# Kernel optimization log

Hardware: AMD Instinct MI355X
Metric: run time of the kernel (lower is better)

The kernel has to match this reference:

```python
import jax, jax.numpy as jnp
import numpy as np
import math

B, S, D = 1, 4096, 2048
H, KVH, HD = 16, 4, 128
ROPE_THETA = 10000.0


def _rope_tables(seq_len, head_dim, theta):
    inv_freq = 1.0 / (theta ** (jnp.arange(0, head_dim, 2, dtype=jnp.float32) / head_dim))
    t = jnp.arange(seq_len, dtype=jnp.float32)
    freqs = jnp.outer(t, inv_freq)                      # [S, HD/2]
    emb = jnp.concatenate([freqs, freqs], axis=-1)      # [S, HD]
    return jnp.cos(emb)[None, None], jnp.sin(emb)[None, None]  # [1,1,S,HD]


def setup_inputs() -> dict:
    key = jax.random.key(0)
    ks = jax.random.split(key, 8)
    hidden_states = jax.random.normal(ks[0], (B, S, D), dtype=jnp.float32)
    # additive causal mask [B,1,S,S]
    neg = jnp.finfo(jnp.float32).min
    causal = jnp.where(jnp.tril(jnp.ones((S, S), dtype=bool)), 0.0, neg)
    attention_mask = jnp.broadcast_to(causal[None, None], (B, 1, S, S)).astype(jnp.float32)
    cos, sin = _rope_tables(S, HD, ROPE_THETA)
    gate = jax.random.uniform(ks[1], (B, S), dtype=jnp.float32, minval=0.05, maxval=1.0)
    sc = lambda fan_in: 1.0 / math.sqrt(fan_in)
    Wq = jax.random.normal(ks[2], (D, H * HD), dtype=jnp.float32) * sc(D)
    Wk = jax.random.normal(ks[3], (D, KVH * HD), dtype=jnp.float32) * sc(D)
    Wv = jax.random.normal(ks[4], (D, KVH * HD), dtype=jnp.float32) * sc(D)
    Wo = jax.random.normal(ks[5], (H * HD, D), dtype=jnp.float32) * sc(H * HD)
    return {"hidden_states": hidden_states, "attention_mask": attention_mask,
            "cos": cos, "sin": sin, "gate": gate,
            "Wq": Wq, "Wk": Wk, "Wv": Wv, "Wo": Wo}


def _rotate_half(x):
    h = x.shape[-1] // 2
    return jnp.concatenate([-x[..., h:], x[..., :h]], axis=-1)


def reference(hidden_states, attention_mask, cos, sin, gate, Wq, Wk, Wv, Wo):
    bsz, q_len, _ = hidden_states.shape
    # projections -> [B, heads, S, HD]
    q = (hidden_states @ Wq).reshape(bsz, q_len, H, HD).transpose(0, 2, 1, 3)
    k = (hidden_states @ Wk).reshape(bsz, q_len, KVH, HD).transpose(0, 2, 1, 3)
    v = (hidden_states @ Wv).reshape(bsz, q_len, KVH, HD).transpose(0, 2, 1, 3)
    # inline RoPE
    q = q * cos + _rotate_half(q) * sin
    k = k * cos + _rotate_half(k) * sin
    # GQA: repeat-interleave kv heads to match q heads
    g = H // KVH
    k = jnp.repeat(k, g, axis=1)
    v = jnp.repeat(v, g, axis=1)
    scores = jnp.einsum('bhqd,bhkd->bhqk', q, k) / math.sqrt(HD)
    scores = scores + attention_mask
    scores = scores + jnp.log(gate + 1e-8)[:, None, None, :]  # gate over kv positions
    weights = jax.nn.softmax(scores.astype(jnp.float32), axis=-1).astype(q.dtype)
    out = jnp.einsum('bhqk,bhkd->bhqd', weights, v)
    out = out.transpose(0, 2, 1, 3).reshape(bsz, q_len, H * HD)
    return out @ Wo
```

## Files before the change

kernel.cpp:

```cpp
#include <hip/hip_runtime.h>
#include <math.h>

#define S_LEN 4096
#define DMODEL 2048
#define NH 16
#define NKVH 4
#define HD 128
#define LDQKV 3072

typedef __attribute__((ext_vector_type(4))) float f32x4;
typedef __attribute__((ext_vector_type(8))) short bf16x8;
typedef __attribute__((ext_vector_type(8))) unsigned short us8;
typedef __attribute__((ext_vector_type(4))) unsigned short us4;

static __device__ __forceinline__ unsigned short f2bf(float f) {
  unsigned int u = __builtin_bit_cast(unsigned int, f);
  u += 0x7fffu + ((u >> 16) & 1u);
  return (unsigned short)(u >> 16);
}
static __device__ __forceinline__ float bf2f(unsigned short h) {
  unsigned int u = ((unsigned int)h) << 16;
  return __builtin_bit_cast(float, u);
}
static __device__ __forceinline__ unsigned int cvt_pk_bf16(float lo, float hi) {
  unsigned int r;
  asm("v_cvt_pk_bf16_f32 %0, %1, %2" : "=v"(r) : "v"(lo), "v"(hi));
  return r;
}

#define GLDS16(g, l) __builtin_amdgcn_global_load_lds( \
    (__attribute__((address_space(1))) void*)(g), \
    (__attribute__((address_space(3))) void*)(l), 16, 0, 0)


__global__ __launch_bounds__(256) void k_prep(
    const float* __restrict__ hid, unsigned short* __restrict__ Xb,
    const float* __restrict__ Wq, const float* __restrict__ Wk,
    const float* __restrict__ Wv, const float* __restrict__ Wo,
    unsigned short* __restrict__ Wt, unsigned short* __restrict__ Wot) {
  __shared__ float tile[64][65];
  const int b = blockIdx.x, t = threadIdx.x;
  if (b < 8192) {
    int i = b * 256 + t;
    const float4* s = (const float4*)hid;
    float4 v = s[i];
    us4 o = { f2bf(v.x), f2bf(v.y), f2bf(v.z), f2bf(v.w) };
    *(us4*)(Xb + (size_t)i * 4) = o;
    return;
  }
  const int bb = b - 8192;
  const float* src;
  unsigned short* dst;
  int N, c;
  if (bb < 1024)      { src = Wq; dst = Wt;                       N = 2048; c = bb; }
  else if (bb < 1280) { src = Wk; dst = Wt + (size_t)2048 * 2048; N = 512;  c = bb - 1024; }
  else if (bb < 1536) { src = Wv; dst = Wt + (size_t)2560 * 2048; N = 512;  c = bb - 1280; }
  else                { src = Wo; dst = Wot;                      N = 2048; c = bb - 1536; }
  const int k0 = (c & 31) * 64, n0 = (c >> 5) * 64;
#pragma unroll
  for (int i = 0; i < 16; ++i) {
    int idx = t + i * 256;
    int r = idx >> 6, cc = idx & 63;
    tile[r][cc] = src[(size_t)(k0 + r) * N + n0 + cc];
  }
  __syncthreads();
#pragma unroll
  for (int i = 0; i < 16; ++i) {
    int idx = t + i * 256;
    int r = idx >> 6, cc = idx & 63;
    dst[(size_t)(n0 + r) * 2048 + k0 + cc] = f2bf(tile[cc][r]);
  }
}


__global__ __launch_bounds__(256) void k_vt(
    const unsigned short* __restrict__ QKV, unsigned short* __restrict__ Vt) {
  __shared__ unsigned short tile[64][72];
  const int b = blockIdx.x, t = threadIdx.x;
  const int s0 = (b & 63) * 64, c0 = (b >> 6) * 64;
#pragma unroll
  for (int i = 0; i < 16; ++i) {
    int idx = t + i * 256;
    int r = idx >> 6, cc = idx & 63;
    tile[r][cc] = QKV[(size_t)(s0 + r) * LDQKV + DMODEL + NKVH * HD + c0 + cc];
  }
  __syncthreads();
#pragma unroll
  for (int i = 0; i < 16; ++i) {
    int idx = t + i * 256;
    int r = idx >> 6, cc = idx & 63;
    int pc = (cc & 3) * 16 + (cc >> 2);
    Vt[(size_t)(c0 + r) * S_LEN + s0 + cc] = tile[pc][r];
  }
}


template<int MODE>
__global__ __launch_bounds__(256) void k_gemm_bt(
    const unsigned short* __restrict__ A, const unsigned short* __restrict__ Bt,
    void* __restrict__ Cp, int M, int N, int K,
    const float* __restrict__ cp, const float* __restrict__ sp) {
  __shared__ __attribute__((aligned(16))) unsigned short As[128 * 32];
  __shared__ __attribute__((aligned(16))) unsigned short Bs[128 * 32];
  const int t = threadIdx.x;
  const int wave = t >> 6, lane = t & 63;
  const int lr = lane & 15, lg = lane >> 4;
  const int bm = blockIdx.x * 128, bn = blockIdx.y * 128;
  const int wr = wave * 32;
  f32x4 acc[2][8];
#pragma unroll
  for (int i = 0; i < 2; ++i)
#pragma unroll
    for (int j = 0; j < 8; ++j) acc[i][j] = (f32x4){0.f, 0.f, 0.f, 0.f};

  for (int k0 = 0; k0 < K; k0 += 32) {
    __syncthreads();
#pragma unroll
    for (int i = 0; i < 2; ++i) {
      const int cb = (wave * 2 + i) * 64;
      const int c = cb + lane;
      const int row = c >> 2, kc = c & 3;
      const int ksw = (kc ^ (row & 3)) * 8;
      GLDS16(A + (size_t)(bm + row) * K + k0 + ksw, (char*)As + cb * 16);
      GLDS16(Bt + (size_t)(bn + row) * K + k0 + ksw, (char*)Bs + cb * 16);
    }
    asm volatile("s_waitcnt vmcnt(0)" ::: "memory");
    __syncthreads();
    bf16x8 af[2], bfr[8];
#pragma unroll
    for (int mi = 0; mi < 2; ++mi) {
      const int row = wr + mi * 16 + lr;
      af[mi] = *(const bf16x8*)(As + row * 32 + ((lg ^ (lr & 3)) * 8));
    }
#pragma unroll
    for (int ni = 0; ni < 8; ++ni) {
      const int row = ni * 16 + lr;
      bfr[ni] = *(const bf16x8*)(Bs + row * 32 + ((lg ^ (lr & 3)) * 8));
    }
#pragma unroll
    for (int mi = 0; mi < 2; ++mi)
#pragma unroll
      for (int ni = 0; ni < 8; ++ni)
        acc[mi][ni] = __builtin_amdgcn_mfma_f32_16x16x32_bf16(af[mi], bfr[ni], acc[mi][ni], 0, 0, 0);
  }

  if (MODE == 1 && bn < NKVH * HD + DMODEL) {
    const float qs = bn < DMODEL ? 0.12751589341664477f : 1.0f;
    unsigned short* o = (unsigned short*)Cp;
#pragma unroll
    for (int mi = 0; mi < 2; ++mi)
#pragma unroll
      for (int r = 0; r < 4; ++r) {
        const int m = bm + wr + mi * 16 + lg * 4 + r;
#pragma unroll
        for (int ni = 0; ni < 4; ++ni) {
          const int d = ni * 16 + lr;
          const float c = cp[m * HD + d], s = sp[m * HD + d];
          const float x1 = acc[mi][ni][r], x2 = acc[mi][ni + 4][r];
          o[(size_t)m * N + bn + d]      = f2bf((x1 * c - x2 * s) * qs);
          o[(size_t)m * N + bn + d + 64] = f2bf((x2 * c + x1 * s) * qs);
        }
      }
    return;
  }
#pragma unroll
  for (int mi = 0; mi < 2; ++mi)
#pragma unroll
    for (int ni = 0; ni < 8; ++ni)
#pragma unroll
      for (int r = 0; r < 4; ++r) {
        const int m = bm + wr + mi * 16 + lg * 4 + r;
        const int n = bn + ni * 16 + lr;
        if (MODE == 2) ((float*)Cp)[(size_t)m * N + n] = acc[mi][ni][r];
        else ((unsigned short*)Cp)[(size_t)m * N + n] = f2bf(acc[mi][ni][r]);
      }
}


#define STAGE_KV(kt_, buf_) do { \
  const int kv0_ = (kt_) * 64; \
  _Pragma("unroll") \
  for (int i_ = 0; i_ < 2; ++i_) { \
    const int cb_ = (wave * 2 + i_) * 64; \
    const int c_ = cb_ + lane; \
    { const int row_ = c_ >> 4, kc_ = c_ & 15; \
      GLDS16(Kp + (size_t)(kv0_ + row_) * LDQKV + ((kc_ ^ (row_ & 7)) * 8), \
             (char*)Ks[buf_] + cb_ * 16); } \
    { const int d_ = c_ >> 3, kc_ = c_ & 7; \
      GLDS16(Vp + (size_t)d_ * S_LEN + kv0_ + ((kc_ ^ (d_ & 7)) * 8), \
             (char*)Vs[buf_] + cb_ * 16); } \
  } \
} while (0)

__global__ __launch_bounds__(512) void k_attn(
    const unsigned short* __restrict__ QKV, const unsigned short* __restrict__ Vt,
    const float* __restrict__ gate, unsigned short* __restrict__ N1,
    unsigned short* __restrict__ N2, float2* __restrict__ Ms) {
  __shared__ __attribute__((aligned(16))) unsigned short Ks[2][64 * 128];
  __shared__ __attribute__((aligned(16))) unsigned short Vs[2][128 * 64];
  __shared__ __attribute__((aligned(16))) unsigned short Ps[8][2][16][72];
  const int bx = blockIdx.x;
  const int st = 15 - (bx >> 5);
  const int rem = bx & 31;
  const int h = rem >> 1, chunk = rem & 1;
  const int kvh = h >> 2;
  const int t = threadIdx.x, wave = t >> 6, lane = t & 63;
  const int lr = lane & 15, lg = lane >> 4;
  const unsigned short* Qp = QKV + h * HD;
  const unsigned short* Kp = QKV + DMODEL + kvh * HD;
  const unsigned short* Vp = Vt + (size_t)kvh * HD * S_LEN;
  bf16x8 vb_ones;
  {
    const short one = (short)0x3F80, z = 0;
    const short e = (lr == 0) ? one : z;
    vb_ones = (bf16x8){e, e, e, e, e, e, e, e};
  }

  const int q0 = st * 256;
  const int half_nt = 2 * st + 2;
  const int kt_lo = chunk * half_nt, kt_hi = kt_lo + half_nt;
  const int qb[2] = { q0 + wave * 32 + lg * 4, q0 + wave * 32 + 16 + lg * 4 };

  bf16x8 qf[2][4];
#pragma unroll
  for (int g = 0; g < 2; ++g) {
    const size_t qoff = (size_t)(q0 + wave * 32 + g * 16 + lr) * LDQKV;
#pragma unroll
    for (int ks = 0; ks < 4; ++ks)
      qf[g][ks] = *(const bf16x8*)(Qp + qoff + ks * 32 + lg * 8);
  }
  f32x4 acc[2][8];
#pragma unroll
  for (int g = 0; g < 2; ++g)
#pragma unroll
    for (int j = 0; j < 8; ++j) acc[g][j] = (f32x4){0.f, 0.f, 0.f, 0.f};
  f32x4 acc_s[2] = { (f32x4){0.f, 0.f, 0.f, 0.f}, (f32x4){0.f, 0.f, 0.f, 0.f} };
  float mrow[2][4] = { {-3e38f, -3e38f, -3e38f, -3e38f}, {-3e38f, -3e38f, -3e38f, -3e38f} };
  f32x4 sc[2][4];
  float g4[4];

  STAGE_KV(kt_lo, kt_lo & 1);

  for (int kt = kt_lo; kt < kt_hi; ++kt) {
    const int kv0 = kt * 64;
    if (kt + 1 < kt_hi) {
      STAGE_KV(kt + 1, (kt + 1) & 1);
      asm volatile("s_waitcnt vmcnt(4)" ::: "memory");
    } else {
      asm volatile("s_waitcnt vmcnt(0)" ::: "memory");
    }
    __builtin_amdgcn_s_barrier();
    const unsigned short* Kb = Ks[kt & 1];
    const unsigned short* Vb = Vs[kt & 1];
#pragma unroll
    for (int cf = 0; cf < 4; ++cf) g4[cf] = gate[kv0 + cf * 16 + lr];

    __builtin_amdgcn_s_setprio(1);
#pragma unroll
    for (int cf = 0; cf < 4; ++cf) {
      sc[0][cf] = (f32x4){0.f, 0.f, 0.f, 0.f};
      sc[1][cf] = (f32x4){0.f, 0.f, 0.f, 0.f};
      const int row = cf * 16 + lr;
#pragma unroll
      for (int ks = 0; ks < 4; ++ks) {
        bf16x8 kb = *(const bf16x8*)(Kb + row * 128 + (((ks * 4 + lg) ^ (lr & 7)) * 8));
        sc[0][cf] = __builtin_amdgcn_mfma_f32_16x16x32_bf16(qf[0][ks], kb, sc[0][cf], 0, 0, 0);
        sc[1][cf] = __builtin_amdgcn_mfma_f32_16x16x32_bf16(qf[1][ks], kb, sc[1][cf], 0, 0, 0);
      }
    }
    __builtin_amdgcn_s_setprio(0);

    const bool tail = kv0 >= q0;
#pragma unroll
    for (int g = 0; g < 2; ++g) {
      if (tail) {
#pragma unroll
        for (int cf = 0; cf < 4; ++cf) {
          const int kpos = kv0 + cf * 16 + lr;
#pragma unroll
          for (int r = 0; r < 4; ++r)
            sc[g][cf][r] = (kpos <= qb[g] + r) ? sc[g][cf][r] : -3e38f;
        }
      }
      float lmax[4];
#pragma unroll
      for (int r = 0; r < 4; ++r)
        lmax[r] = fmaxf(fmaxf(sc[g][0][r], sc[g][1][r]), fmaxf(sc[g][2][r], sc[g][3][r]));
      bool need = (lmax[0] > mrow[g][0] + 11.5416f) | (lmax[1] > mrow[g][1] + 11.5416f) |
                  (lmax[2] > mrow[g][2] + 11.5416f) | (lmax[3] > mrow[g][3] + 11.5416f);
      if (__any(need)) {
        float tm[4] = {lmax[0], lmax[1], lmax[2], lmax[3]};
#pragma unroll
        for (int off = 8; off; off >>= 1)
#pragma unroll
          for (int r = 0; r < 4; ++r) tm[r] = fmaxf(tm[r], __shfl_xor(tm[r], off));
#pragma unroll
        for (int r = 0; r < 4; ++r) {
          const float mn = fmaxf(mrow[g][r], tm[r]);
          const float alpha = __builtin_amdgcn_exp2f(mrow[g][r] - mn);
          mrow[g][r] = mn;
#pragma unroll
          for (int j = 0; j < 8; ++j) acc[g][j][r] *= alpha;
          acc_s[g][r] *= alpha;
        }
      }
#pragma unroll
      for (int r = 0; r < 4; ++r) {
        float p0 = __builtin_amdgcn_exp2f(sc[g][0][r] - mrow[g][r]) * g4[0];
        float p1 = __builtin_amdgcn_exp2f(sc[g][1][r] - mrow[g][r]) * g4[1];
        float p2 = __builtin_amdgcn_exp2f(sc[g][2][r] - mrow[g][r]) * g4[2];
        float p3 = __builtin_amdgcn_exp2f(sc[g][3][r] - mrow[g][r]) * g4[3];
        uint2 pk = { cvt_pk_bf16(p0, p1), cvt_pk_bf16(p2, p3) };
        *(uint2*)(&Ps[wave][g][lg * 4 + r][lr * 4]) = pk;
      }
    }
    __builtin_amdgcn_s_setprio(1);
#pragma unroll
    for (int ks = 0; ks < 2; ++ks) {
      bf16x8 pa0 = *(const bf16x8*)(&Ps[wave][0][lr][ks * 32 + lg * 8]);
      bf16x8 pa1 = *(const bf16x8*)(&Ps[wave][1][lr][ks * 32 + lg * 8]);
#pragma unroll
      for (int j = 0; j < 8; ++j) {
        const int d = j * 16 + lr;
        bf16x8 vb = *(const bf16x8*)(Vb + d * 64 + (((ks * 4 + lg) ^ (lr & 7)) * 8));
        acc[0][j] = __builtin_amdgcn_mfma_f32_16x16x32_bf16(pa0, vb, acc[0][j], 0, 0, 0);
        acc[1][j] = __builtin_amdgcn_mfma_f32_16x16x32_bf16(pa1, vb, acc[1][j], 0, 0, 0);
      }
      acc_s[0] = __builtin_amdgcn_mfma_f32_16x16x32_bf16(pa0, vb_ones, acc_s[0], 0, 0, 0);
      acc_s[1] = __builtin_amdgcn_mfma_f32_16x16x32_bf16(pa1, vb_ones, acc_s[1], 0, 0, 0);
    }
    __builtin_amdgcn_s_setprio(0);
    __builtin_amdgcn_s_barrier();
  }

  unsigned short* Nd = chunk ? N2 : N1;
#pragma unroll
  for (int g = 0; g < 2; ++g) {
#pragma unroll
    for (int j = 0; j < 8; ++j)
#pragma unroll
      for (int r = 0; r < 4; ++r)
        Nd[(size_t)(qb[g] + r) * DMODEL + h * HD + j * 16 + lr] = f2bf(acc[g][j][r]);
  }
  if (lr == 0) {
#pragma unroll
    for (int g = 0; g < 2; ++g)
#pragma unroll
      for (int r = 0; r < 4; ++r)
        Ms[(size_t)(chunk * 16 + h) * S_LEN + qb[g] + r] =
            make_float2(mrow[g][r], acc_s[g][r]);
  }
}


__global__ __launch_bounds__(256) void k_comb(
    unsigned short* __restrict__ N1, const unsigned short* __restrict__ N2,
    const float2* __restrict__ Ms) {
  const int gid = blockIdx.x * 256 + threadIdx.x;
  const size_t e = (size_t)gid * 8;
  const int row = (int)(e >> 11);
  const int col = (int)(e & 2047);
  const int h = col >> 7;
  const float2 a = Ms[(size_t)h * S_LEN + row];
  const float2 b = Ms[(size_t)(16 + h) * S_LEN + row];
  const float m = fmaxf(a.x, b.x);
  const float w1 = __builtin_amdgcn_exp2f(a.x - m);
  const float w2 = __builtin_amdgcn_exp2f(b.x - m);
  const float inv = 1.0f / (w1 * a.y + w2 * b.y);
  us8 n1 = *(const us8*)(N1 + e);
  us8 n2 = *(const us8*)(N2 + e);
  us8 o;
#pragma unroll
  for (int k = 0; k < 8; ++k)
    o[k] = f2bf((w1 * bf2f(n1[k]) + w2 * bf2f(n2[k])) * inv);
  *(us8*)(N1 + e) = o;
}


extern "C" void kernel_launch(void* const* d_in, const int* in_sizes, int n_in,
                              void* d_out, int out_size, void* d_ws, size_t ws_size,
                              hipStream_t stream) {
  (void)in_sizes; (void)n_in; (void)out_size; (void)ws_size;
  const float* hid  = (const float*)d_in[0];
  const float* cosp = (const float*)d_in[2];
  const float* sinp = (const float*)d_in[3];
  const float* gate = (const float*)d_in[4];
  const float* Wq   = (const float*)d_in[5];
  const float* Wk   = (const float*)d_in[6];
  const float* Wv   = (const float*)d_in[7];
  const float* Wo   = (const float*)d_in[8];
  float* out = (float*)d_out;
  char* ws = (char*)d_ws;
  unsigned short* Xb   = (unsigned short*)(ws);
  unsigned short* Wt   = (unsigned short*)(ws + (size_t)16777216);
  unsigned short* Wot  = (unsigned short*)(ws + (size_t)29360128);
  unsigned short* QKV  = (unsigned short*)(ws + (size_t)37748736);
  unsigned short* Oatt = (unsigned short*)(ws + (size_t)62914560);
  unsigned short* Vt   = (unsigned short*)(ws + (size_t)79691776);
  unsigned short* Np   = Xb;
  float2* Ms           = (float2*)Wt;

  k_prep<<<10752, 256, 0, stream>>>(hid, Xb, Wq, Wk, Wv, Wo, Wt, Wot);
  k_gemm_bt<1><<<dim3(32, 24), 256, 0, stream>>>(Xb, Wt, QKV, 4096, 3072, 2048, cosp, sinp);
  k_vt<<<512, 256, 0, stream>>>(QKV, Vt);
  k_attn<<<512, 512, 0, stream>>>(QKV, Vt, gate, Oatt, Np, Ms);
  k_comb<<<4096, 256, 0, stream>>>(Oatt, Np, Ms);
  k_gemm_bt<2><<<dim3(32, 16), 256, 0, stream>>>(Oatt, Wot, out, 4096, 2048, 2048, nullptr, nullptr);
}
```

Baseline: 247.1 us.

## Rewrite projection GEMMs with triple-buffered 256x128 tiles and 8-wave ping-pong scheduling

Replaces the single-buffered 128x128, 4-wave GEMM with a 256x128-tile, 8-wave kernel. It uses a 3-stage LDS ring with BK=64, so global-to-LDS loads for tile k+2 overlap the MFMA work on tile k, along with s_setprio around the MFMA bursts and an XCD-aware block remapping. The goal is to hide global load latency and drop the per-iteration full vmcnt(0) stall of the old loop. The cost is 144KB of LDS, which allows one workgroup per CU, and a more intricate barrier and waitcnt protocol.

```diff
diff --git a/kernel.cpp b/kernel.cpp
--- a/kernel.cpp
+++ b/kernel.cpp
@@ -95,53 +95,91 @@
 }
 
 
+#define STG_A(kt_, buf_, j_) do { \
+  const int row_ = (j_) * 64 + srow; \
+  GLDS16(A + (size_t)(bm + row_) * K + (kt_) * 64 + ((gsel ^ (srow & 7)) * 8), \
+         (char*)Ab[buf_] + (j_) * 8192 + wave * 1024); \
+} while (0)
+#define STG_B(kt_, buf_, j_) do { \
+  const int row_ = (j_) * 64 + srow; \
+  GLDS16(Bt + (size_t)(bn + row_) * K + (kt_) * 64 + ((gsel ^ (srow & 7)) * 8), \
+         (char*)Bb[buf_] + (j_) * 8192 + wave * 1024); \
+} while (0)
+
 template<int MODE>
-__global__ __launch_bounds__(256) void k_gemm_bt(
+__global__ __launch_bounds__(512, 1) void k_gemm8(
     const unsigned short* __restrict__ A, const unsigned short* __restrict__ Bt,
-    void* __restrict__ Cp, int M, int N, int K,
+    void* __restrict__ Cp, int M, int N, int K, int nbm, int nbn,
     const float* __restrict__ cp, const float* __restrict__ sp) {
-  __shared__ __attribute__((aligned(16))) unsigned short As[128 * 32];
-  __shared__ __attribute__((aligned(16))) unsigned short Bs[128 * 32];
-  const int t = threadIdx.x;
-  const int wave = t >> 6, lane = t & 63;
+  __shared__ __attribute__((aligned(16))) unsigned short Ab[3][256 * 64];
+  __shared__ __attribute__((aligned(16))) unsigned short Bb[3][128 * 64];
+  const int t = threadIdx.x, wave = t >> 6, lane = t & 63;
   const int lr = lane & 15, lg = lane >> 4;
-  const int bm = blockIdx.x * 128, bn = blockIdx.y * 128;
+  const int srow = wave * 8 + (lane >> 3);
+  const int gsel = lane & 7;
+  const int nwg = nbm * nbn;
+  const int q8 = nwg >> 3;
+  const int wg = (blockIdx.x & 7) * q8 + (blockIdx.x >> 3);
+  const int bm = (wg % nbm) * 256, bn = (wg / nbm) * 128;
   const int wr = wave * 32;
+
   f32x4 acc[2][8];
 #pragma unroll
   for (int i = 0; i < 2; ++i)
 #pragma unroll
     for (int j = 0; j < 8; ++j) acc[i][j] = (f32x4){0.f, 0.f, 0.f, 0.f};
 
-  for (int k0 = 0; k0 < K; k0 += 32) {
-    __syncthreads();
-#pragma unroll
-    for (int i = 0; i < 2; ++i) {
-      const int cb = (wave * 2 + i) * 64;
-      const int c = cb + lane;
-      const int row = c >> 2, kc = c & 3;
-      const int ksw = (kc ^ (row & 3)) * 8;
-      GLDS16(A + (size_t)(bm + row) * K + k0 + ksw, (char*)As + cb * 16);
-      GLDS16(Bt + (size_t)(bn + row) * K + k0 + ksw, (char*)Bs + cb * 16);
-    }
-    asm volatile("s_waitcnt vmcnt(0)" ::: "memory");
-    __syncthreads();
-    bf16x8 af[2], bfr[8];
-#pragma unroll
-    for (int mi = 0; mi < 2; ++mi) {
-      const int row = wr + mi * 16 + lr;
-      af[mi] = *(const bf16x8*)(As + row * 32 + ((lg ^ (lr & 3)) * 8));
-    }
-#pragma unroll
-    for (int ni = 0; ni < 8; ++ni) {
-      const int row = ni * 16 + lr;
-      bfr[ni] = *(const bf16x8*)(Bs + row * 32 + ((lg ^ (lr & 3)) * 8));
-    }
-#pragma unroll
-    for (int mi = 0; mi < 2; ++mi)
-#pragma unroll
-      for (int ni = 0; ni < 8; ++ni)
-        acc[mi][ni] = __builtin_amdgcn_mfma_f32_16x16x32_bf16(af[mi], bfr[ni], acc[mi][ni], 0, 0, 0);
+#pragma unroll
+  for (int tt = 0; tt < 2; ++tt) {
+    STG_A(tt, tt, 0); STG_A(tt, tt, 1); STG_A(tt, tt, 2); STG_A(tt, tt, 3);
+    STG_B(tt, tt, 0); STG_B(tt, tt, 1);
+  }
+  asm volatile("s_waitcnt vmcnt(6)" ::: "memory");
+  __builtin_amdgcn_s_barrier();
+
+  const int nkt = K >> 6;
+  for (int kt = 0; kt < nkt; ++kt) {
+    const int cur = kt % 3;
+    const int nx = (kt + 2) % 3;
+    const unsigned short* Ac = Ab[cur];
+    const unsigned short* Bc = Bb[cur];
+    const bool stg = kt < nkt - 2;
+
+    bf16x8 aq[2], bq[8][2];
+#pragma unroll
+    for (int ks = 0; ks < 2; ++ks)
+      aq[ks] = *(const bf16x8*)(Ac + (wr + lr) * 64 + (((ks * 4 + lg) ^ (lr & 7)) * 8));
+#pragma unroll
+    for (int nf = 0; nf < 8; ++nf)
+#pragma unroll
+      for (int ks = 0; ks < 2; ++ks)
+        bq[nf][ks] = *(const bf16x8*)(Bc + (nf * 16 + lr) * 64 + (((ks * 4 + lg) ^ (lr & 7)) * 8));
+    if (stg) { STG_A(kt + 2, nx, 0); STG_A(kt + 2, nx, 1); STG_B(kt + 2, nx, 0); }
+    __builtin_amdgcn_s_barrier();
+    __builtin_amdgcn_s_setprio(1);
+#pragma unroll
+    for (int nf = 0; nf < 8; ++nf)
+#pragma unroll
+      for (int ks = 0; ks < 2; ++ks)
+        acc[0][nf] = __builtin_amdgcn_mfma_f32_16x16x32_bf16(aq[ks], bq[nf][ks], acc[0][nf], 0, 0, 0);
+    __builtin_amdgcn_s_setprio(0);
+    __builtin_amdgcn_s_barrier();
+
+#pragma unroll
+    for (int ks = 0; ks < 2; ++ks)
+      aq[ks] = *(const bf16x8*)(Ac + (wr + 16 + lr) * 64 + (((ks * 4 + lg) ^ (lr & 7)) * 8));
+    if (stg) { STG_A(kt + 2, nx, 2); STG_A(kt + 2, nx, 3); STG_B(kt + 2, nx, 1); }
+    __builtin_amdgcn_s_barrier();
+    __builtin_amdgcn_s_setprio(1);
+#pragma unroll
+    for (int nf = 0; nf < 8; ++nf)
+#pragma unroll
+      for (int ks = 0; ks < 2; ++ks)
+        acc[1][nf] = __builtin_amdgcn_mfma_f32_16x16x32_bf16(aq[ks], bq[nf][ks], acc[1][nf], 0, 0, 0);
+    __builtin_amdgcn_s_setprio(0);
+    if (stg)                  asm volatile("s_waitcnt vmcnt(6)" ::: "memory");
+    else if (kt == nkt - 2)   asm volatile("s_waitcnt vmcnt(0)" ::: "memory");
+    __builtin_amdgcn_s_barrier();
   }
 
   if (MODE == 1 && bn < NKVH * HD + DMODEL) {
@@ -401,9 +439,9 @@
   float2* Ms           = (float2*)Wt;
 
   k_prep<<<10752, 256, 0, stream>>>(hid, Xb, Wq, Wk, Wv, Wo, Wt, Wot);
-  k_gemm_bt<1><<<dim3(32, 24), 256, 0, stream>>>(Xb, Wt, QKV, 4096, 3072, 2048, cosp, sinp);
+  k_gemm8<1><<<384, 512, 0, stream>>>(Xb, Wt, QKV, 4096, 3072, 2048, 16, 24, cosp, sinp);
   k_vt<<<512, 256, 0, stream>>>(QKV, Vt);
   k_attn<<<512, 512, 0, stream>>>(QKV, Vt, gate, Oatt, Np, Ms);
   k_comb<<<4096, 256, 0, stream>>>(Oatt, Np, Ms);
-  k_gemm_bt<2><<<dim3(32, 16), 256, 0, stream>>>(Oatt, Wot, out, 4096, 2048, 2048, nullptr, nullptr);
-}
+  k_gemm8<2><<<256, 512, 0, stream>>>(Oatt, Wot, out, 4096, 2048, 2048, 16, 16, nullptr, nullptr);
+}
```

Measured after the change: 257.2 us. 4.1% more time.

## Fold gate into V transpose and row-sum MFMA instead of per-tile multiply

Applied to the files above, without the earlier changes.

Multiplies V by the per-position gate while building the transposed V, and writes a permuted bf16 gate array that is staged into shared memory once per attention block. The softmax denominator MFMA then uses the gate fragment in place of the ones vector, so the per-tile gate loads and per-element multiplies on probabilities are removed. In exchange, V is rounded to bf16 after gating (extra rounding), more LDS is used, and there is an extra small load per k-step.

```diff
diff --git a/kernel.cpp b/kernel.cpp
--- a/kernel.cpp
+++ b/kernel.cpp
@@ -74,23 +74,31 @@
 
 
 __global__ __launch_bounds__(256) void k_vt(
-    const unsigned short* __restrict__ QKV, unsigned short* __restrict__ Vt) {
+    const unsigned short* __restrict__ QKV, const float* __restrict__ gate,
+    unsigned short* __restrict__ Vt, unsigned short* __restrict__ garr) {
   __shared__ unsigned short tile[64][72];
   const int b = blockIdx.x, t = threadIdx.x;
-  const int s0 = (b & 63) * 64, c0 = (b >> 6) * 64;
-#pragma unroll
-  for (int i = 0; i < 16; ++i) {
-    int idx = t + i * 256;
-    int r = idx >> 6, cc = idx & 63;
-    tile[r][cc] = QKV[(size_t)(s0 + r) * LDQKV + DMODEL + NKVH * HD + c0 + cc];
-  }
-  __syncthreads();
-#pragma unroll
-  for (int i = 0; i < 16; ++i) {
-    int idx = t + i * 256;
-    int r = idx >> 6, cc = idx & 63;
-    int pc = (cc & 3) * 16 + (cc >> 2);
-    Vt[(size_t)(c0 + r) * S_LEN + s0 + cc] = tile[pc][r];
+  if (b < 512) {
+    const int s0 = (b & 63) * 64, c0 = (b >> 6) * 64;
+#pragma unroll
+    for (int i = 0; i < 16; ++i) {
+      int idx = t + i * 256;
+      int r = idx >> 6, cc = idx & 63;
+      tile[r][cc] = QKV[(size_t)(s0 + r) * LDQKV + DMODEL + NKVH * HD + c0 + cc];
+    }
+    __syncthreads();
+#pragma unroll
+    for (int i = 0; i < 16; ++i) {
+      int idx = t + i * 256;
+      int r = idx >> 6, cc = idx & 63;
+      int pc = (cc & 3) * 16 + (cc >> 2);
+      float gv = bf2f(tile[pc][r]) * gate[s0 + pc];
+      Vt[(size_t)(c0 + r) * S_LEN + s0 + cc] = f2bf(gv);
+    }
+  } else {
+    int gid = (b - 512) * 256 + t;
+    int blk = gid >> 6, c = gid & 63;
+    garr[gid] = f2bf(gate[blk * 64 + (c & 3) * 16 + (c >> 2)]);
   }
 }
 
@@ -194,11 +202,12 @@
 
 __global__ __launch_bounds__(512) void k_attn(
     const unsigned short* __restrict__ QKV, const unsigned short* __restrict__ Vt,
-    const float* __restrict__ gate, unsigned short* __restrict__ N1,
+    const unsigned short* __restrict__ garr, unsigned short* __restrict__ N1,
     unsigned short* __restrict__ N2, float2* __restrict__ Ms) {
   __shared__ __attribute__((aligned(16))) unsigned short Ks[2][64 * 128];
   __shared__ __attribute__((aligned(16))) unsigned short Vs[2][128 * 64];
   __shared__ __attribute__((aligned(16))) unsigned short Ps[8][2][16][72];
+  __shared__ __attribute__((aligned(16))) unsigned short Lg[4096];
   const int bx = blockIdx.x;
   const int st = 15 - (bx >> 5);
   const int rem = bx & 31;
@@ -209,12 +218,8 @@
   const unsigned short* Qp = QKV + h * HD;
   const unsigned short* Kp = QKV + DMODEL + kvh * HD;
   const unsigned short* Vp = Vt + (size_t)kvh * HD * S_LEN;
-  bf16x8 vb_ones;
-  {
-    const short one = (short)0x3F80, z = 0;
-    const short e = (lr == 0) ? one : z;
-    vb_ones = (bf16x8){e, e, e, e, e, e, e, e};
-  }
+
+  GLDS16(garr + wave * 512 + lane * 8, (char*)Lg + wave * 1024);
 
   const int q0 = st * 256;
   const int half_nt = 2 * st + 2;
@@ -237,7 +242,6 @@
   f32x4 acc_s[2] = { (f32x4){0.f, 0.f, 0.f, 0.f}, (f32x4){0.f, 0.f, 0.f, 0.f} };
   float mrow[2][4] = { {-3e38f, -3e38f, -3e38f, -3e38f}, {-3e38f, -3e38f, -3e38f, -3e38f} };
   f32x4 sc[2][4];
-  float g4[4];
 
   STAGE_KV(kt_lo, kt_lo & 1);
 
@@ -252,8 +256,6 @@
     __builtin_amdgcn_s_barrier();
     const unsigned short* Kb = Ks[kt & 1];
     const unsigned short* Vb = Vs[kt & 1];
-#pragma unroll
-    for (int cf = 0; cf < 4; ++cf) g4[cf] = gate[kv0 + cf * 16 + lr];
 
     __builtin_amdgcn_s_setprio(1);
 #pragma unroll
@@ -306,10 +308,10 @@
       }
 #pragma unroll
       for (int r = 0; r < 4; ++r) {
-        float p0 = __builtin_amdgcn_exp2f(sc[g][0][r] - mrow[g][r]) * g4[0];
-        float p1 = __builtin_amdgcn_exp2f(sc[g][1][r] - mrow[g][r]) * g4[1];
-        float p2 = __builtin_amdgcn_exp2f(sc[g][2][r] - mrow[g][r]) * g4[2];
-        float p3 = __builtin_amdgcn_exp2f(sc[g][3][r] - mrow[g][r]) * g4[3];
+        float p0 = __builtin_amdgcn_exp2f(sc[g][0][r] - mrow[g][r]);
+        float p1 = __builtin_amdgcn_exp2f(sc[g][1][r] - mrow[g][r]);
+        float p2 = __builtin_amdgcn_exp2f(sc[g][2][r] - mrow[g][r]);
+        float p3 = __builtin_amdgcn_exp2f(sc[g][3][r] - mrow[g][r]);
         uint2 pk = { cvt_pk_bf16(p0, p1), cvt_pk_bf16(p2, p3) };
         *(uint2*)(&Ps[wave][g][lg * 4 + r][lr * 4]) = pk;
       }
@@ -319,6 +321,8 @@
     for (int ks = 0; ks < 2; ++ks) {
       bf16x8 pa0 = *(const bf16x8*)(&Ps[wave][0][lr][ks * 32 + lg * 8]);
       bf16x8 pa1 = *(const bf16x8*)(&Ps[wave][1][lr][ks * 32 + lg * 8]);
+      bf16x8 gfrag = (bf16x8){0, 0, 0, 0, 0, 0, 0, 0};
+      if (lr == 0) gfrag = *(const bf16x8*)(Lg + kv0 + ks * 32 + lg * 8);
 #pragma unroll
       for (int j = 0; j < 8; ++j) {
         const int d = j * 16 + lr;
@@ -326,8 +330,8 @@
         acc[0][j] = __builtin_amdgcn_mfma_f32_16x16x32_bf16(pa0, vb, acc[0][j], 0, 0, 0);
         acc[1][j] = __builtin_amdgcn_mfma_f32_16x16x32_bf16(pa1, vb, acc[1][j], 0, 0, 0);
       }
-      acc_s[0] = __builtin_amdgcn_mfma_f32_16x16x32_bf16(pa0, vb_ones, acc_s[0], 0, 0, 0);
-      acc_s[1] = __builtin_amdgcn_mfma_f32_16x16x32_bf16(pa1, vb_ones, acc_s[1], 0, 0, 0);
+      acc_s[0] = __builtin_amdgcn_mfma_f32_16x16x32_bf16(pa0, gfrag, acc_s[0], 0, 0, 0);
+      acc_s[1] = __builtin_amdgcn_mfma_f32_16x16x32_bf16(pa1, gfrag, acc_s[1], 0, 0, 0);
     }
     __builtin_amdgcn_s_setprio(0);
     __builtin_amdgcn_s_barrier();
@@ -399,11 +403,12 @@
   unsigned short* Vt   = (unsigned short*)(ws + (size_t)79691776);
   unsigned short* Np   = Xb;
   float2* Ms           = (float2*)Wt;
+  unsigned short* garr = (unsigned short*)(ws + (size_t)18874368);
 
   k_prep<<<10752, 256, 0, stream>>>(hid, Xb, Wq, Wk, Wv, Wo, Wt, Wot);
   k_gemm_bt<1><<<dim3(32, 24), 256, 0, stream>>>(Xb, Wt, QKV, 4096, 3072, 2048, cosp, sinp);
-  k_vt<<<512, 256, 0, stream>>>(QKV, Vt);
-  k_attn<<<512, 512, 0, stream>>>(QKV, Vt, gate, Oatt, Np, Ms);
+  k_vt<<<528, 256, 0, stream>>>(QKV, gate, Vt, garr);
+  k_attn<<<512, 512, 0, stream>>>(QKV, Vt, garr, Oatt, Np, Ms);
   k_comb<<<4096, 256, 0, stream>>>(Oatt, Np, Ms);
   k_gemm_bt<2><<<dim3(32, 16), 256, 0, stream>>>(Oatt, Wot, out, 4096, 2048, 2048, nullptr, nullptr);
 }
```

After: 243.5 us. No clear change (-1.4%).
